# Optimization experiments

Hardware: AMD Instinct MI355X
Metric: run time of the kernel (lower is better)

## Reference

```python
import jax, jax.numpy as jnp
import numpy as np

B, D, H, W = 8, 64, 128, 64
DX = (2.0 - -0.5) / 63.0
DY = (0.5 - -0.5) / 127.0
DZ = (0.3 - -0.5) / 63.0
INV_RE = 1.0 / 1000000.0
U_INF = 1.0
L_FIELD, L_CT = 1.0, 10.0
L_CONT, L_MOM = 1.0, 1.0
L_NOSLIP, L_INLET, L_OUTLET = 10.0, 5.0, 1.0

# central first differences
def _ddx(f, d):  # along W (last dim)
    return (f[..., 2:] - f[..., :-2]) / (2.0 * d)

def _ddy(f, d):  # along H
    return (f[..., 2:, :] - f[..., :-2, :]) / (2.0 * d)

def _ddz(f, d):  # along D
    return (f[..., 2:, :, :] - f[..., :-2, :, :]) / (2.0 * d)

# second differences
def _lap_x(f, d):
    return (f[..., 2:] - 2.0 * f[..., 1:-1] + f[..., :-2]) / (d * d)

def _lap_y(f, d):
    return (f[..., 2:, :] - 2.0 * f[..., 1:-1, :] + f[..., :-2, :]) / (d * d)

def _lap_z(f, d):
    return (f[..., 2:, :, :] - 2.0 * f[..., 1:-1, :, :] + f[..., :-2, :, :]) / (d * d)

# trims: after an x-stencil we still need to trim D,H (etc.) so every
# derivative ends up on the common interior grid (D-2, H-2, W-2)
def _tx(f):
    return f[:, :, 1:-1, 1:-1, :]

def _ty(f):
    return f[:, :, 1:-1, :, 1:-1]

def _tz(f):
    return f[:, :, :, 1:-1, 1:-1]

def _tin(f):
    return f[:, :, 1:-1, 1:-1, 1:-1]


def setup_inputs() -> dict:
    key = jax.random.key(0)
    k1, k2, k3, k4, k5 = jax.random.split(key, 5)
    return {
        "field": jax.random.normal(k1, (B, 4, D, H, W), dtype=jnp.float32),
        "ct": jax.random.normal(k2, (B, 1), dtype=jnp.float32),
        "gt_field": jax.random.normal(k3, (B, 4, D, H, W), dtype=jnp.float32),
        "gt_ct": jax.random.normal(k4, (B, 1), dtype=jnp.float32),
        "sdf": jax.random.normal(k5, (B, 1, D, H, W), dtype=jnp.float32),
    }


def _total_loss(field, ct, gt_field, gt_ct, sdf):
    # --- supervised terms ---
    loss_field = jnp.mean((field - gt_field) ** 2)
    loss_ct = jnp.mean((ct - gt_ct) ** 2)

    u = field[:, 0:1]
    v = field[:, 1:2]
    w = field[:, 2:3]
    p = field[:, 3:4]

    # --- physics: continuity ---
    du_dx = _tx(_ddx(u, DX))
    dv_dy = _ty(_ddy(v, DY))
    dw_dz = _tz(_ddz(w, DZ))
    div = du_dx + dv_dy + dw_dz
    fluid = (_tin(sdf) > 0).astype(field.dtype)
    loss_cont = jnp.mean((div * fluid) ** 2)

    # --- physics: momentum ---
    u_i, v_i, w_i = _tin(u), _tin(v), _tin(w)
    du_dy = _ty(_ddy(u, DY)); du_dz = _tz(_ddz(u, DZ))
    dv_dx = _tx(_ddx(v, DX)); dv_dz = _tz(_ddz(v, DZ))
    dw_dx = _tx(_ddx(w, DX)); dw_dy = _ty(_ddy(w, DY))
    dp_dx = _tx(_ddx(p, DX)); dp_dy = _ty(_ddy(p, DY)); dp_dz = _tz(_ddz(p, DZ))
    lap_u = _tx(_lap_x(u, DX)) + _ty(_lap_y(u, DY)) + _tz(_lap_z(u, DZ))
    lap_v = _tx(_lap_x(v, DX)) + _ty(_lap_y(v, DY)) + _tz(_lap_z(v, DZ))
    lap_w = _tx(_lap_x(w, DX)) + _ty(_lap_y(w, DY)) + _tz(_lap_z(w, DZ))
    res_x = u_i * du_dx + v_i * du_dy + w_i * du_dz + dp_dx - INV_RE * lap_u
    res_y = u_i * dv_dx + v_i * dv_dy + w_i * dv_dz + dp_dy - INV_RE * lap_v
    res_z = u_i * dw_dx + v_i * dw_dy + w_i * dw_dz + dp_dz - INV_RE * lap_w
    loss_mom = jnp.mean((res_x * fluid) ** 2 + (res_y * fluid) ** 2 + (res_z * fluid) ** 2)

    # --- boundary terms ---
    solid = (sdf <= 0).astype(field.dtype)
    loss_noslip = jnp.mean((u ** 2 + v ** 2 + w ** 2) * solid)
    loss_inlet = (
        jnp.mean((u[:, :, :, :, 0] - U_INF) ** 2)
        + jnp.mean(v[:, :, :, :, 0] ** 2)
        + jnp.mean(w[:, :, :, :, 0] ** 2)
    )
    loss_outlet = (
        jnp.mean((u[:, :, :, :, -1] - u[:, :, :, :, -2]) ** 2)
        + jnp.mean((v[:, :, :, :, -1] - v[:, :, :, :, -2]) ** 2)
        + jnp.mean((w[:, :, :, :, -1] - w[:, :, :, :, -2]) ** 2)
    )

    total = (
        L_FIELD * loss_field
        + L_CT * loss_ct
        + L_CONT * loss_cont
        + L_MOM * loss_mom
        + L_NOSLIP * loss_noslip
        + L_INLET * loss_inlet
        + L_OUTLET * loss_outlet
    )
    return total


def reference(field, ct, gt_field, gt_ct, sdf):
    return _total_loss(field, ct, gt_field, gt_ct, sdf)
```

## Files before the change

### kernel.cpp

```cpp
#include <hip/hip_runtime.h>

constexpr int Bn = 8, Dn = 64, Hn = 128, Wn = 64;
constexpr int sH = Wn;
constexpr int sD = Hn * Wn;
constexpr int sC = Dn * Hn * Wn;
constexpr int sB = 4 * sC;

constexpr double DXd = (2.0 - -0.5) / 63.0;
constexpr double DYd = (0.5 - -0.5) / 127.0;
constexpr double DZd = (0.3 - -0.5) / 63.0;

constexpr float I2DX = (float)(0.5 / DXd);
constexpr float I2DY = (float)(0.5 / DYd);
constexpr float I2DZ = (float)(0.5 / DZd);
constexpr float IDX2 = (float)(1.0 / (DXd * DXd));
constexpr float IDY2 = (float)(1.0 / (DYd * DYd));
constexpr float IDZ2 = (float)(1.0 / (DZd * DZd));
constexpr float INV_RE = 1.0e-6f;

constexpr float CF  = (float)(1.0  / (8.0 * 4.0 * 64.0 * 128.0 * 64.0));
constexpr float CCT = (float)(10.0 / 8.0);
constexpr float CCM = (float)(1.0  / (8.0 * 62.0 * 126.0 * 62.0));
constexpr float CN  = (float)(10.0 / (8.0 * 64.0 * 128.0 * 64.0));
constexpr float CI  = (float)(5.0  / (8.0 * 64.0 * 128.0));
constexpr float CO  = (float)(1.0  / (8.0 * 64.0 * 128.0));

__device__ __forceinline__ float4 ld4(const float* __restrict__ p, int off) {
    return *reinterpret_cast<const float4*>(p + off);
}

__global__ __launch_bounds__(256) void fno3d_loss_kernel(
    const float* __restrict__ field,
    const float* __restrict__ ct,
    const float* __restrict__ gt_field,
    const float* __restrict__ gt_ct,
    const float* __restrict__ sdf,
    float* __restrict__ out)
{
    const int x  = threadIdx.x;
    const int ty = threadIdx.y;
    const int tz = threadIdx.z;
    const int h  = blockIdx.y * 4 + ty;
    const int bdt = blockIdx.z;
    const int b  = bdt >> 4;
    const int d  = (bdt & 15) * 4 + tz;
    const int w0 = x * 4;

    const float* Fb = field    + b * sB;
    const float* Gb = gt_field + b * sB;
    const float* Sb = sdf      + b * sC;

    const int ctr = d * sD + h * sH + w0;
    const int hm = (h > 0)      ? h - 1 : h;
    const int hp = (h < Hn - 1) ? h + 1 : h;
    const int dm = (d > 0)      ? d - 1 : d;
    const int dp = (d < Dn - 1) ? d + 1 : d;
    const int oyp = d * sD + hp * sH + w0;
    const int oym = d * sD + hm * sH + w0;
    const int ozp = dp * sD + h * sH + w0;
    const int ozm = dm * sD + h * sH + w0;

    const float4 cu = ld4(Fb, ctr);
    const float4 cv = ld4(Fb, sC + ctr);
    const float4 cw = ld4(Fb, 2 * sC + ctr);
    const float4 cp = ld4(Fb, 3 * sC + ctr);

    const float4 gu = ld4(Gb, ctr);
    const float4 gv = ld4(Gb, sC + ctr);
    const float4 gw = ld4(Gb, 2 * sC + ctr);
    const float4 gp = ld4(Gb, 3 * sC + ctr);

    const float4 sv = ld4(Sb, ctr);

    const float4 uyp = ld4(Fb, oyp),          uym = ld4(Fb, oym);
    const float4 vyp = ld4(Fb, sC + oyp),     vym = ld4(Fb, sC + oym);
    const float4 wyp = ld4(Fb, 2 * sC + oyp), wym = ld4(Fb, 2 * sC + oym);
    const float4 pyp = ld4(Fb, 3 * sC + oyp), pym = ld4(Fb, 3 * sC + oym);

    const float4 uzp = ld4(Fb, ozp),          uzm = ld4(Fb, ozm);
    const float4 vzp = ld4(Fb, sC + ozp),     vzm = ld4(Fb, sC + ozm);
    const float4 wzp = ld4(Fb, 2 * sC + ozp), wzm = ld4(Fb, 2 * sC + ozm);
    const float4 pzp = ld4(Fb, 3 * sC + ozp), pzm = ld4(Fb, 3 * sC + ozm);

    const float uLs = __shfl_up(cu.w, 1), uRs = __shfl_down(cu.x, 1);
    const float vLs = __shfl_up(cv.w, 1), vRs = __shfl_down(cv.x, 1);
    const float wLs = __shfl_up(cw.w, 1), wRs = __shfl_down(cw.x, 1);
    const float pLs = __shfl_up(cp.w, 1), pRs = __shfl_down(cp.x, 1);

    const float* au  = reinterpret_cast<const float*>(&cu);
    const float* av  = reinterpret_cast<const float*>(&cv);
    const float* aw  = reinterpret_cast<const float*>(&cw);
    const float* ap  = reinterpret_cast<const float*>(&cp);
    const float* agu = reinterpret_cast<const float*>(&gu);
    const float* agv = reinterpret_cast<const float*>(&gv);
    const float* agw = reinterpret_cast<const float*>(&gw);
    const float* agp = reinterpret_cast<const float*>(&gp);
    const float* as_ = reinterpret_cast<const float*>(&sv);
    const float* auyp = reinterpret_cast<const float*>(&uyp);
    const float* auym = reinterpret_cast<const float*>(&uym);
    const float* avyp = reinterpret_cast<const float*>(&vyp);
    const float* avym = reinterpret_cast<const float*>(&vym);
    const float* awyp = reinterpret_cast<const float*>(&wyp);
    const float* awym = reinterpret_cast<const float*>(&wym);
    const float* apyp = reinterpret_cast<const float*>(&pyp);
    const float* apym = reinterpret_cast<const float*>(&pym);
    const float* auzp = reinterpret_cast<const float*>(&uzp);
    const float* auzm = reinterpret_cast<const float*>(&uzm);
    const float* avzp = reinterpret_cast<const float*>(&vzp);
    const float* avzm = reinterpret_cast<const float*>(&vzm);
    const float* awzp = reinterpret_cast<const float*>(&wzp);
    const float* awzm = reinterpret_cast<const float*>(&wzm);
    const float* apzp = reinterpret_cast<const float*>(&pzp);
    const float* apzm = reinterpret_cast<const float*>(&pzm);

    const bool hIn = (h >= 1) & (h <= Hn - 2);
    const bool dIn = (d >= 1) & (d <= Dn - 2);

    float acc = 0.f;

    #pragma unroll
    for (int e = 0; e < 4; ++e) {
        const int w = w0 + e;
        const float u = au[e], v = av[e], wq = aw[e], pq = ap[e];

        {
            const float d0 = u  - agu[e];
            const float d1 = v  - agv[e];
            const float d2 = wq - agw[e];
            const float d3 = pq - agp[e];
            acc += CF * (d0 * d0 + d1 * d1 + d2 * d2 + d3 * d3);
        }

        const float s = as_[e];

        acc += ((s <= 0.f) ? CN : 0.f) * (u * u + v * v + wq * wq);

        {
            const float du = u - 1.0f;
            acc += ((w == 0) ? CI : 0.f) * (du * du + v * v + wq * wq);
        }

        const float uxm = (e == 0) ? uLs : au[e - 1];
        const float uxp = (e == 3) ? uRs : au[e + 1];
        const float vxm = (e == 0) ? vLs : av[e - 1];
        const float vxp = (e == 3) ? vRs : av[e + 1];
        const float wxm = (e == 0) ? wLs : aw[e - 1];
        const float wxp = (e == 3) ? wRs : aw[e + 1];
        const float pxm = (e == 0) ? pLs : ap[e - 1];
        const float pxp = (e == 3) ? pRs : ap[e + 1];

        const float du_dx = (uxp - uxm) * I2DX;
        const float du_dy = (auyp[e] - auym[e]) * I2DY;
        const float du_dz = (auzp[e] - auzm[e]) * I2DZ;
        const float dv_dx = (vxp - vxm) * I2DX;
        const float dv_dy = (avyp[e] - avym[e]) * I2DY;
        const float dv_dz = (avzp[e] - avzm[e]) * I2DZ;
        const float dw_dx = (wxp - wxm) * I2DX;
        const float dw_dy = (awyp[e] - awym[e]) * I2DY;
        const float dw_dz = (awzp[e] - awzm[e]) * I2DZ;
        const float dp_dx = (pxp - pxm) * I2DX;
        const float dp_dy = (apyp[e] - apym[e]) * I2DY;
        const float dp_dz = (apzp[e] - apzm[e]) * I2DZ;

        const float div = du_dx + dv_dy + dw_dz;

        const float lap_u = (uxp - 2.f * u  + uxm) * IDX2 + (auyp[e] - 2.f * u  + auym[e]) * IDY2 + (auzp[e] - 2.f * u  + auzm[e]) * IDZ2;
        const float lap_v = (vxp - 2.f * v  + vxm) * IDX2 + (avyp[e] - 2.f * v  + avym[e]) * IDY2 + (avzp[e] - 2.f * v  + avzm[e]) * IDZ2;
        const float lap_w = (wxp - 2.f * wq + wxm) * IDX2 + (awyp[e] - 2.f * wq + awym[e]) * IDY2 + (awzp[e] - 2.f * wq + awzm[e]) * IDZ2;

        const float rx = u * du_dx + v * du_dy + wq * du_dz + dp_dx - INV_RE * lap_u;
        const float ry = u * dv_dx + v * dv_dy + wq * dv_dz + dp_dy - INV_RE * lap_v;
        const float rz = u * dw_dx + v * dw_dy + wq * dw_dz + dp_dz - INV_RE * lap_w;

        const bool wIn = (w >= 1) & (w <= Wn - 2);
        const float m = (s > 0.f && wIn && hIn && dIn) ? CCM : 0.f;
        acc += m * (div * div + rx * rx + ry * ry + rz * rz);
    }

    if (x == 15) {
        const float a0 = au[3] - au[2];
        const float a1 = av[3] - av[2];
        const float a2 = aw[3] - aw[2];
        acc += CO * (a0 * a0 + a1 * a1 + a2 * a2);
    }

    if (blockIdx.y == 0 && blockIdx.z == 0 &&
        threadIdx.x == 0 && threadIdx.y == 0 && threadIdx.z == 0) {
        float t = 0.f;
        for (int i = 0; i < Bn; ++i) {
            const float dc = ct[i] - gt_ct[i];
            t += dc * dc;
        }
        acc += CCT * t;
    }

    for (int off = 32; off > 0; off >>= 1)
        acc += __shfl_down(acc, off);

    __shared__ float wsum[4];
    const int tid  = (threadIdx.z * 4 + threadIdx.y) * 16 + threadIdx.x;
    const int wid  = tid >> 6;
    const int lane = tid & 63;
    if (lane == 0) wsum[wid] = acc;
    __syncthreads();
    if (tid == 0)
        atomicAdd(out, wsum[0] + wsum[1] + wsum[2] + wsum[3]);
}

extern "C" void kernel_launch(void* const* d_in, const int* in_sizes, int n_in,
                              void* d_out, int out_size, void* d_ws, size_t ws_size,
                              hipStream_t stream) {
    const float* field    = (const float*)d_in[0];
    const float* ct       = (const float*)d_in[1];
    const float* gt_field = (const float*)d_in[2];
    const float* gt_ct    = (const float*)d_in[3];
    const float* sdf      = (const float*)d_in[4];
    float* out = (float*)d_out;

    hipMemsetAsync(out, 0, (size_t)out_size * sizeof(float), stream);

    dim3 block(16, 4, 4);
    dim3 grid(1, Hn / 4, (Dn / 4) * Bn);
    hipLaunchKernelGGL(fno3d_loss_kernel, grid, block, 0, stream,
                       field, ct, gt_field, gt_ct, sdf, out);
}
```

Before: 180.0 us.

## March along depth with register-rotated z-neighbours and two-pass deterministic reduction

Each block now walks 8 depth slices per thread and keeps the previous, current and next slices of u,v,w,p in registers, so z-neighbour loads are reused instead of re-fetched for each voxel. Blocks shrink to 128 threads with launch_bounds(128,2), and the grid becomes a flat 1024 blocks. The global atomicAdd and memset are replaced by per-block partials written to the workspace, which a second single-block kernel sums and then adds the ct loss. This cuts redundant loads but lowers parallelism, adds register pressure and costs an extra kernel launch.

```diff
diff --git a/kernel.cpp b/kernel.cpp
--- a/kernel.cpp
+++ b/kernel.cpp
@@ -3,12 +3,12 @@
 constexpr int Bn = 8, Dn = 64, Hn = 128, Wn = 64;
 constexpr int sH = Wn;
 constexpr int sD = Hn * Wn;
-constexpr int sC = Dn * Hn * Wn;
+constexpr int sC = Dn * sD;
 constexpr int sB = 4 * sC;
 
-constexpr double DXd = (2.0 - -0.5) / 63.0;
-constexpr double DYd = (0.5 - -0.5) / 127.0;
-constexpr double DZd = (0.3 - -0.5) / 63.0;
+constexpr double DXd = 2.5 / 63.0;
+constexpr double DYd = 1.0 / 127.0;
+constexpr double DZd = 0.8 / 63.0;
 
 constexpr float I2DX = (float)(0.5 / DXd);
 constexpr float I2DY = (float)(0.5 / DYd);
@@ -29,182 +29,207 @@
     return *reinterpret_cast<const float4*>(p + off);
 }
 
-__global__ __launch_bounds__(256) void fno3d_loss_kernel(
+__global__ __launch_bounds__(128, 2) void fno3d_main(
     const float* __restrict__ field,
-    const float* __restrict__ ct,
     const float* __restrict__ gt_field,
-    const float* __restrict__ gt_ct,
     const float* __restrict__ sdf,
-    float* __restrict__ out)
+    float* __restrict__ partials)
 {
-    const int x  = threadIdx.x;
-    const int ty = threadIdx.y;
-    const int tz = threadIdx.z;
-    const int h  = blockIdx.y * 4 + ty;
-    const int bdt = blockIdx.z;
-    const int b  = bdt >> 4;
-    const int d  = (bdt & 15) * 4 + tz;
-    const int w0 = x * 4;
+    const int x   = threadIdx.x;
+    const int ty  = threadIdx.y;
+    const int blk = blockIdx.x;
+    const int b   = blk >> 7;
+    const int rem = blk & 127;
+    const int d0  = (rem >> 4) << 3;
+    const int h   = ((rem & 15) << 3) + ty;
+    const int w0  = x << 2;
 
     const float* Fb = field    + b * sB;
     const float* Gb = gt_field + b * sB;
     const float* Sb = sdf      + b * sC;
 
-    const int ctr = d * sD + h * sH + w0;
     const int hm = (h > 0)      ? h - 1 : h;
     const int hp = (h < Hn - 1) ? h + 1 : h;
-    const int dm = (d > 0)      ? d - 1 : d;
-    const int dp = (d < Dn - 1) ? d + 1 : d;
-    const int oyp = d * sD + hp * sH + w0;
-    const int oym = d * sD + hm * sH + w0;
-    const int ozp = dp * sD + h * sH + w0;
-    const int ozm = dm * sD + h * sH + w0;
-
-    const float4 cu = ld4(Fb, ctr);
-    const float4 cv = ld4(Fb, sC + ctr);
-    const float4 cw = ld4(Fb, 2 * sC + ctr);
-    const float4 cp = ld4(Fb, 3 * sC + ctr);
-
-    const float4 gu = ld4(Gb, ctr);
-    const float4 gv = ld4(Gb, sC + ctr);
-    const float4 gw = ld4(Gb, 2 * sC + ctr);
-    const float4 gp = ld4(Gb, 3 * sC + ctr);
-
-    const float4 sv = ld4(Sb, ctr);
-
-    const float4 uyp = ld4(Fb, oyp),          uym = ld4(Fb, oym);
-    const float4 vyp = ld4(Fb, sC + oyp),     vym = ld4(Fb, sC + oym);
-    const float4 wyp = ld4(Fb, 2 * sC + oyp), wym = ld4(Fb, 2 * sC + oym);
-    const float4 pyp = ld4(Fb, 3 * sC + oyp), pym = ld4(Fb, 3 * sC + oym);
-
-    const float4 uzp = ld4(Fb, ozp),          uzm = ld4(Fb, ozm);
-    const float4 vzp = ld4(Fb, sC + ozp),     vzm = ld4(Fb, sC + ozm);
-    const float4 wzp = ld4(Fb, 2 * sC + ozp), wzm = ld4(Fb, 2 * sC + ozm);
-    const float4 pzp = ld4(Fb, 3 * sC + ozp), pzm = ld4(Fb, 3 * sC + ozm);
-
-    const float uLs = __shfl_up(cu.w, 1), uRs = __shfl_down(cu.x, 1);
-    const float vLs = __shfl_up(cv.w, 1), vRs = __shfl_down(cv.x, 1);
-    const float wLs = __shfl_up(cw.w, 1), wRs = __shfl_down(cw.x, 1);
-    const float pLs = __shfl_up(cp.w, 1), pRs = __shfl_down(cp.x, 1);
-
-    const float* au  = reinterpret_cast<const float*>(&cu);
-    const float* av  = reinterpret_cast<const float*>(&cv);
-    const float* aw  = reinterpret_cast<const float*>(&cw);
-    const float* ap  = reinterpret_cast<const float*>(&cp);
-    const float* agu = reinterpret_cast<const float*>(&gu);
-    const float* agv = reinterpret_cast<const float*>(&gv);
-    const float* agw = reinterpret_cast<const float*>(&gw);
-    const float* agp = reinterpret_cast<const float*>(&gp);
-    const float* as_ = reinterpret_cast<const float*>(&sv);
-    const float* auyp = reinterpret_cast<const float*>(&uyp);
-    const float* auym = reinterpret_cast<const float*>(&uym);
-    const float* avyp = reinterpret_cast<const float*>(&vyp);
-    const float* avym = reinterpret_cast<const float*>(&vym);
-    const float* awyp = reinterpret_cast<const float*>(&wyp);
-    const float* awym = reinterpret_cast<const float*>(&wym);
-    const float* apyp = reinterpret_cast<const float*>(&pyp);
-    const float* apym = reinterpret_cast<const float*>(&pym);
-    const float* auzp = reinterpret_cast<const float*>(&uzp);
-    const float* auzm = reinterpret_cast<const float*>(&uzm);
-    const float* avzp = reinterpret_cast<const float*>(&vzp);
-    const float* avzm = reinterpret_cast<const float*>(&vzm);
-    const float* awzp = reinterpret_cast<const float*>(&wzp);
-    const float* awzm = reinterpret_cast<const float*>(&wzm);
-    const float* apzp = reinterpret_cast<const float*>(&pzp);
-    const float* apzm = reinterpret_cast<const float*>(&pzm);
-
     const bool hIn = (h >= 1) & (h <= Hn - 2);
-    const bool dIn = (d >= 1) & (d <= Dn - 2);
+
+    const int rowc = h  * sH + w0;
+    const int rowm = hm * sH + w0;
+    const int rowp = hp * sH + w0;
+
+    const int dm0 = (d0 > 0) ? d0 - 1 : 0;
+    const int dn0 = (d0 < Dn - 1) ? d0 + 1 : d0;
+
+    float4 pU = ld4(Fb, dm0 * sD + rowc);
+    float4 pV = ld4(Fb, sC + dm0 * sD + rowc);
+    float4 pW = ld4(Fb, 2 * sC + dm0 * sD + rowc);
+    float4 cU = ld4(Fb, d0 * sD + rowc);
+    float4 cV = ld4(Fb, sC + d0 * sD + rowc);
+    float4 cW = ld4(Fb, 2 * sC + d0 * sD + rowc);
+    float4 cP = ld4(Fb, 3 * sC + d0 * sD + rowc);
+    float4 nU = ld4(Fb, dn0 * sD + rowc);
+    float4 nV = ld4(Fb, sC + dn0 * sD + rowc);
+    float4 nW = ld4(Fb, 2 * sC + dn0 * sD + rowc);
+    float4 nP = ld4(Fb, 3 * sC + dn0 * sD + rowc);
+    float4 pP = ld4(Fb, 3 * sC + dm0 * sD + rowc);
+
+    float4 cGU = ld4(Gb, d0 * sD + rowc);
+    float4 cGV = ld4(Gb, sC + d0 * sD + rowc);
+    float4 cGW = ld4(Gb, 2 * sC + d0 * sD + rowc);
+    float4 cGP = ld4(Gb, 3 * sC + d0 * sD + rowc);
+    float4 cS  = ld4(Sb, d0 * sD + rowc);
 
     float acc = 0.f;
 
     #pragma unroll
-    for (int e = 0; e < 4; ++e) {
-        const int w = w0 + e;
-        const float u = au[e], v = av[e], wq = aw[e], pq = ap[e];
-
-        {
-            const float d0 = u  - agu[e];
-            const float d1 = v  - agv[e];
-            const float d2 = wq - agw[e];
-            const float d3 = pq - agp[e];
-            acc += CF * (d0 * d0 + d1 * d1 + d2 * d2 + d3 * d3);
+    for (int k = 0; k < 8; ++k) {
+        const int d   = d0 + k;
+        const int dn  = (d < Dn - 1) ? d + 1 : d;
+        const int dnn = (dn < Dn - 1) ? dn + 1 : dn;
+
+        const float4 qU = ld4(Fb, dnn * sD + rowc);
+        const float4 qV = ld4(Fb, sC + dnn * sD + rowc);
+        const float4 qW = ld4(Fb, 2 * sC + dnn * sD + rowc);
+        const float4 qP = ld4(Fb, 3 * sC + dnn * sD + rowc);
+        const float4 nGU = ld4(Gb, dn * sD + rowc);
+        const float4 nGV = ld4(Gb, sC + dn * sD + rowc);
+        const float4 nGW = ld4(Gb, 2 * sC + dn * sD + rowc);
+        const float4 nGP = ld4(Gb, 3 * sC + dn * sD + rowc);
+        const float4 nS  = ld4(Sb, dn * sD + rowc);
+
+        const float4 uym = ld4(Fb, d * sD + rowm), uyp = ld4(Fb, d * sD + rowp);
+        const float4 vym = ld4(Fb, sC + d * sD + rowm), vyp = ld4(Fb, sC + d * sD + rowp);
+        const float4 wym = ld4(Fb, 2 * sC + d * sD + rowm), wyp = ld4(Fb, 2 * sC + d * sD + rowp);
+        const float4 pym = ld4(Fb, 3 * sC + d * sD + rowm), pyp = ld4(Fb, 3 * sC + d * sD + rowp);
+
+        const float uLs = __shfl_up(cU.w, 1), uRs = __shfl_down(cU.x, 1);
+        const float vLs = __shfl_up(cV.w, 1), vRs = __shfl_down(cV.x, 1);
+        const float wLs = __shfl_up(cW.w, 1), wRs = __shfl_down(cW.x, 1);
+        const float pLs = __shfl_up(cP.w, 1), pRs = __shfl_down(cP.x, 1);
+
+        const float* au = (const float*)&cU; const float* av = (const float*)&cV;
+        const float* aw = (const float*)&cW; const float* ap = (const float*)&cP;
+        const float* apu = (const float*)&pU; const float* apv = (const float*)&pV;
+        const float* apw = (const float*)&pW; const float* app = (const float*)&pP;
+        const float* anu = (const float*)&nU; const float* anv = (const float*)&nV;
+        const float* anw = (const float*)&nW; const float* anp = (const float*)&nP;
+        const float* agu = (const float*)&cGU; const float* agv = (const float*)&cGV;
+        const float* agw = (const float*)&cGW; const float* agp = (const float*)&cGP;
+        const float* as_ = (const float*)&cS;
+        const float* ayum = (const float*)&uym; const float* ayup = (const float*)&uyp;
+        const float* ayvm = (const float*)&vym; const float* ayvp = (const float*)&vyp;
+        const float* aywm = (const float*)&wym; const float* aywp = (const float*)&wyp;
+        const float* aypm = (const float*)&pym; const float* aypp = (const float*)&pyp;
+
+        const bool dIn = (d >= 1) & (d <= Dn - 2);
+
+        #pragma unroll
+        for (int e = 0; e < 4; ++e) {
+            const int w = w0 + e;
+            const float u = au[e], v = av[e], wq = aw[e], pq = ap[e];
+
+            {
+                const float e0 = u  - agu[e];
+                const float e1 = v  - agv[e];
+                const float e2 = wq - agw[e];
+                const float e3 = pq - agp[e];
+                acc += CF * (e0 * e0 + e1 * e1 + e2 * e2 + e3 * e3);
+            }
+
+            const float s = as_[e];
+
+            acc += ((s <= 0.f) ? CN : 0.f) * (u * u + v * v + wq * wq);
+
+            {
+                const float du = u - 1.0f;
+                acc += ((w == 0) ? CI : 0.f) * (du * du + v * v + wq * wq);
+            }
+
+            const float uxm = (e == 0) ? uLs : au[e - 1];
+            const float uxp = (e == 3) ? uRs : au[e + 1];
+            const float vxm = (e == 0) ? vLs : av[e - 1];
+            const float vxp = (e == 3) ? vRs : av[e + 1];
+            const float wxm = (e == 0) ? wLs : aw[e - 1];
+            const float wxp = (e == 3) ? wRs : aw[e + 1];
+            const float pxm = (e == 0) ? pLs : ap[e - 1];
+            const float pxp = (e == 3) ? pRs : ap[e + 1];
+
+            const float du_dx = (uxp - uxm) * I2DX;
+            const float du_dy = (ayup[e] - ayum[e]) * I2DY;
+            const float du_dz = (anu[e] - apu[e]) * I2DZ;
+            const float dv_dx = (vxp - vxm) * I2DX;
+            const float dv_dy = (ayvp[e] - ayvm[e]) * I2DY;
+            const float dv_dz = (anv[e] - apv[e]) * I2DZ;
+            const float dw_dx = (wxp - wxm) * I2DX;
+            const float dw_dy = (aywp[e] - aywm[e]) * I2DY;
+            const float dw_dz = (anw[e] - apw[e]) * I2DZ;
+            const float dp_dx = (pxp - pxm) * I2DX;
+            const float dp_dy = (aypp[e] - aypm[e]) * I2DY;
+            const float dp_dz = (anp[e] - app[e]) * I2DZ;
+
+            const float div = du_dx + dv_dy + dw_dz;
+
+            const float lap_u = (uxp - 2.f * u  + uxm) * IDX2 + (ayup[e] - 2.f * u  + ayum[e]) * IDY2 + (anu[e] - 2.f * u  + apu[e]) * IDZ2;
+            const float lap_v = (vxp - 2.f * v  + vxm) * IDX2 + (ayvp[e] - 2.f * v  + ayvm[e]) * IDY2 + (anv[e] - 2.f * v  + apv[e]) * IDZ2;
+            const float lap_w = (wxp - 2.f * wq + wxm) * IDX2 + (aywp[e] - 2.f * wq + aywm[e]) * IDY2 + (anw[e] - 2.f * wq + apw[e]) * IDZ2;
+
+            const float rx = u * du_dx + v * du_dy + wq * du_dz + dp_dx - INV_RE * lap_u;
+            const float ry = u * dv_dx + v * dv_dy + wq * dv_dz + dp_dy - INV_RE * lap_v;
+            const float rz = u * dw_dx + v * dw_dy + wq * dw_dz + dp_dz - INV_RE * lap_w;
+
+            const bool wIn = (w >= 1) & (w <= Wn - 2);
+            const float m = (s > 0.f && wIn && hIn && dIn) ? CCM : 0.f;
+            acc += m * (div * div + rx * rx + ry * ry + rz * rz);
         }
 
-        const float s = as_[e];
-
-        acc += ((s <= 0.f) ? CN : 0.f) * (u * u + v * v + wq * wq);
-
-        {
-            const float du = u - 1.0f;
-            acc += ((w == 0) ? CI : 0.f) * (du * du + v * v + wq * wq);
+        if (x == 15) {
+            const float a0 = au[3] - au[2];
+            const float a1 = av[3] - av[2];
+            const float a2 = aw[3] - aw[2];
+            acc += CO * (a0 * a0 + a1 * a1 + a2 * a2);
         }
 
-        const float uxm = (e == 0) ? uLs : au[e - 1];
-        const float uxp = (e == 3) ? uRs : au[e + 1];
-        const float vxm = (e == 0) ? vLs : av[e - 1];
-        const float vxp = (e == 3) ? vRs : av[e + 1];
-        const float wxm = (e == 0) ? wLs : aw[e - 1];
-        const float wxp = (e == 3) ? wRs : aw[e + 1];
-        const float pxm = (e == 0) ? pLs : ap[e - 1];
-        const float pxp = (e == 3) ? pRs : ap[e + 1];
-
-        const float du_dx = (uxp - uxm) * I2DX;
-        const float du_dy = (auyp[e] - auym[e]) * I2DY;
-        const float du_dz = (auzp[e] - auzm[e]) * I2DZ;
-        const float dv_dx = (vxp - vxm) * I2DX;
-        const float dv_dy = (avyp[e] - avym[e]) * I2DY;
-        const float dv_dz = (avzp[e] - avzm[e]) * I2DZ;
-        const float dw_dx = (wxp - wxm) * I2DX;
-        const float dw_dy = (awyp[e] - awym[e]) * I2DY;
-        const float dw_dz = (awzp[e] - awzm[e]) * I2DZ;
-        const float dp_dx = (pxp - pxm) * I2DX;
-        const float dp_dy = (apyp[e] - apym[e]) * I2DY;
-        const float dp_dz = (apzp[e] - apzm[e]) * I2DZ;
-
-        const float div = du_dx + dv_dy + dw_dz;
-
-        const float lap_u = (uxp - 2.f * u  + uxm) * IDX2 + (auyp[e] - 2.f * u  + auym[e]) * IDY2 + (auzp[e] - 2.f * u  + auzm[e]) * IDZ2;
-        const float lap_v = (vxp - 2.f * v  + vxm) * IDX2 + (avyp[e] - 2.f * v  + avym[e]) * IDY2 + (avzp[e] - 2.f * v  + avzm[e]) * IDZ2;
-        const float lap_w = (wxp - 2.f * wq + wxm) * IDX2 + (awyp[e] - 2.f * wq + awym[e]) * IDY2 + (awzp[e] - 2.f * wq + awzm[e]) * IDZ2;
-
-        const float rx = u * du_dx + v * du_dy + wq * du_dz + dp_dx - INV_RE * lap_u;
-        const float ry = u * dv_dx + v * dv_dy + wq * dv_dz + dp_dy - INV_RE * lap_v;
-        const float rz = u * dw_dx + v * dw_dy + wq * dw_dz + dp_dz - INV_RE * lap_w;
-
-        const bool wIn = (w >= 1) & (w <= Wn - 2);
-        const float m = (s > 0.f && wIn && hIn && dIn) ? CCM : 0.f;
-        acc += m * (div * div + rx * rx + ry * ry + rz * rz);
-    }
-
-    if (x == 15) {
-        const float a0 = au[3] - au[2];
-        const float a1 = av[3] - av[2];
-        const float a2 = aw[3] - aw[2];
-        acc += CO * (a0 * a0 + a1 * a1 + a2 * a2);
-    }
-
-    if (blockIdx.y == 0 && blockIdx.z == 0 &&
-        threadIdx.x == 0 && threadIdx.y == 0 && threadIdx.z == 0) {
-        float t = 0.f;
-        for (int i = 0; i < Bn; ++i) {
-            const float dc = ct[i] - gt_ct[i];
-            t += dc * dc;
-        }
-        acc += CCT * t;
+        pU = cU; pV = cV; pW = cW; pP = cP;
+        cU = nU; cV = nV; cW = nW; cP = nP;
+        nU = qU; nV = qV; nW = qW; nP = qP;
+        cGU = nGU; cGV = nGV; cGW = nGW; cGP = nGP;
+        cS = nS;
     }
 
     for (int off = 32; off > 0; off >>= 1)
         acc += __shfl_down(acc, off);
 
-    __shared__ float wsum[4];
-    const int tid  = (threadIdx.z * 4 + threadIdx.y) * 16 + threadIdx.x;
+    __shared__ float wsum[2];
+    const int tid  = threadIdx.y * 16 + threadIdx.x;
     const int wid  = tid >> 6;
     const int lane = tid & 63;
     if (lane == 0) wsum[wid] = acc;
     __syncthreads();
-    if (tid == 0)
-        atomicAdd(out, wsum[0] + wsum[1] + wsum[2] + wsum[3]);
+    if (tid == 0) partials[blk] = wsum[0] + wsum[1];
+}
+
+__global__ __launch_bounds__(256) void fno3d_reduce(
+    const float* __restrict__ partials,
+    const float* __restrict__ ct,
+    const float* __restrict__ gt_ct,
+    float* __restrict__ out)
+{
+    const int t = threadIdx.x;
+    float s = partials[t] + partials[t + 256] + partials[t + 512] + partials[t + 768];
+    for (int off = 32; off > 0; off >>= 1)
+        s += __shfl_down(s, off);
+
+    __shared__ float wsum[4];
+    if ((t & 63) == 0) wsum[t >> 6] = s;
+    __syncthreads();
+    if (t == 0) {
+        float tot = wsum[0] + wsum[1] + wsum[2] + wsum[3];
+        float ctl = 0.f;
+        for (int i = 0; i < Bn; ++i) {
+            const float dc = ct[i] - gt_ct[i];
+            ctl += dc * dc;
+        }
+        out[0] = tot + CCT * ctl;
+    }
 }
 
 extern "C" void kernel_launch(void* const* d_in, const int* in_sizes, int n_in,
@@ -215,12 +240,11 @@
     const float* gt_field = (const float*)d_in[2];
     const float* gt_ct    = (const float*)d_in[3];
     const float* sdf      = (const float*)d_in[4];
-    float* out = (float*)d_out;
-
-    hipMemsetAsync(out, 0, (size_t)out_size * sizeof(float), stream);
-
-    dim3 block(16, 4, 4);
-    dim3 grid(1, Hn / 4, (Dn / 4) * Bn);
-    hipLaunchKernelGGL(fno3d_loss_kernel, grid, block, 0, stream,
-                       field, ct, gt_field, gt_ct, sdf, out);
-}
+    float* out      = (float*)d_out;
+    float* partials = (float*)d_ws;
+
+    hipLaunchKernelGGL(fno3d_main, dim3(1024), dim3(16, 8, 1), 0, stream,
+                       field, gt_field, sdf, partials);
+    hipLaunchKernelGGL(fno3d_reduce, dim3(1), dim3(256), 0, stream,
+                       partials, ct, gt_ct, out);
+}
```

After: 170.6 us. -5.2%, faster.
